# Kernel optimization log

Measured on AMD Instinct MI355X. Metric: run time of the kernel, lower is better.

Reference implementation:

```python
import jax, jax.numpy as jnp
import numpy as np
import math

BS, LQ, LKV = 4, 2048, 2048
D_LATENT, D_MODEL, HEADS = 512, 512, 8
D_K = D_MODEL // HEADS


def setup_inputs() -> dict:
    key = jax.random.key(0)
    ks = jax.random.split(key, 12)
    s = 0.02
    return {
        "q": jax.random.normal(ks[0], (BS, LQ, D_LATENT), jnp.float32),
        "k": jax.random.normal(ks[1], (BS, LKV, D_MODEL), jnp.float32),
        "v": jax.random.normal(ks[2], (BS, LKV, D_MODEL), jnp.float32),
        "weights": jax.random.uniform(ks[3], (BS, LKV), jnp.float32) + 1e-3,
        "Wq": jax.random.normal(ks[4], (D_LATENT, D_MODEL), jnp.float32) * s,
        "bq": jnp.zeros((D_MODEL,), jnp.float32),
        "Wk": jax.random.normal(ks[5], (D_MODEL, D_MODEL), jnp.float32) * s,
        "bk": jnp.zeros((D_MODEL,), jnp.float32),
        "Wv": jax.random.normal(ks[6], (D_MODEL, D_MODEL), jnp.float32) * s,
        "bv": jnp.zeros((D_MODEL,), jnp.float32),
        "Wo": jax.random.normal(ks[7], (D_MODEL, D_MODEL), jnp.float32) * s,
        "bo": jnp.zeros((D_MODEL,), jnp.float32),
    }


def reference(q, k, v, weights, Wq, bq, Wk, bk, Wv, bv, Wo, bo):
    bs = q.shape[0]
    # QKV projections, split into heads: [bs, h, L, d_k]
    qh = (q @ Wq + bq).reshape(bs, -1, HEADS, D_K).transpose(0, 2, 1, 3)
    kh = (k @ Wk + bk).reshape(bs, -1, HEADS, D_K).transpose(0, 2, 1, 3)
    vh = (v @ Wv + bv).reshape(bs, -1, HEADS, D_K).transpose(0, 2, 1, 3)
    # scaled dot-product scores [bs, h, Lq, Lkv]
    scores = jnp.einsum("bhqd,bhkd->bhqk", qh, kh) / math.sqrt(D_K)
    p = jax.nn.softmax(scores, axis=-1)
    # post-softmax external weight renormalization
    wp = p * weights[:, None, None, :]
    wp = wp / wp.sum(-1, keepdims=True)
    out = jnp.einsum("bhqk,bhkd->bhqd", wp, vh)
    concat = out.transpose(0, 2, 1, 3).reshape(bs, -1, D_MODEL)
    return concat @ Wo + bo
```

## Files before the change

### kernel.cpp

```cpp
#include <hip/hip_runtime.h>
#include <hip/hip_bf16.h>

#define LQ 2048
#define LKV 2048
#define DM 512
#define NH 8
#define DK 64

typedef __attribute__((ext_vector_type(8))) __bf16 bf16x8;
typedef __attribute__((ext_vector_type(4))) float f32x4;
typedef __attribute__((ext_vector_type(16))) float f32x16;

#define AS1 __attribute__((address_space(1)))
#define AS3 __attribute__((address_space(3)))

static __device__ __forceinline__ unsigned short f2bf(float x) {
  unsigned u = __float_as_uint(x);
  return (unsigned short)((u + 0x7fffu + ((u >> 16) & 1u)) >> 16);
}
static __device__ __forceinline__ float bf2f(unsigned short u) {
  return __uint_as_float(((unsigned)u) << 16);
}
static __device__ __forceinline__ bf16x8 cvt8(f32x4 a, f32x4 b) {
  bf16x8 r;
  r[0] = (__bf16)a[0]; r[1] = (__bf16)a[1]; r[2] = (__bf16)a[2]; r[3] = (__bf16)a[3];
  r[4] = (__bf16)b[0]; r[5] = (__bf16)b[1]; r[6] = (__bf16)b[2]; r[7] = (__bf16)b[3];
  return r;
}

__global__ __launch_bounds__(256) void transpose_w(
    const float* __restrict__ Wq, const float* __restrict__ Wk,
    const float* __restrict__ Wv, const float* __restrict__ Wo,
    unsigned short* __restrict__ WtAll)
{
  const float* W = blockIdx.z == 0 ? Wq : blockIdx.z == 1 ? Wk : blockIdx.z == 2 ? Wv : Wo;
  unsigned short* Wt = WtAll + (size_t)blockIdx.z * DM * DM;
  __shared__ float tile[32][33];
  const int t = threadIdx.x;
  const int tr = t >> 3;
  const int tc4 = (t & 7) * 4;
  const int k0 = blockIdx.x * 32, n0 = blockIdx.y * 32;
  float4 v = *(const float4*)(W + (size_t)(k0 + tr) * DM + n0 + tc4);
  tile[tr][tc4 + 0] = v.x; tile[tr][tc4 + 1] = v.y;
  tile[tr][tc4 + 2] = v.z; tile[tr][tc4 + 3] = v.w;
  __syncthreads();
  ushort4 o;
  o.x = f2bf(tile[tc4 + 0][tr]);
  o.y = f2bf(tile[tc4 + 1][tr]);
  o.z = f2bf(tile[tc4 + 2][tr]);
  o.w = f2bf(tile[tc4 + 3][tr]);
  *(ushort4*)(Wt + (size_t)(n0 + tr) * DM + k0 + tc4) = o;
}

__global__ __launch_bounds__(256) void gemm_qkv(
    const float* __restrict__ qin, const float* __restrict__ kin, const float* __restrict__ vin,
    const unsigned short* __restrict__ WtAll,
    const float* __restrict__ bq, const float* __restrict__ bk, const float* __restrict__ bv,
    unsigned short* __restrict__ qh, unsigned short* __restrict__ kh, unsigned short* __restrict__ vh)
{
  const int bid = blockIdx.x;
  const int x = bid & 7, j = bid >> 3;
  const int p = x + 8 * (j >> 2);
  const int nt = j & 3;
  const int mode = p >> 6, mtile = p & 63;

  const float* A = mode == 0 ? qin : (mode == 1 ? kin : vin);
  const unsigned short* Bt = WtAll + (size_t)mode * DM * DM;
  const float* bias = mode == 0 ? bq : (mode == 1 ? bk : bv);
  unsigned short* out = mode == 0 ? qh : (mode == 1 ? kh : vh);
  const float scale = (mode == 0) ? 0.18033688011112042f : 1.0f;

  __shared__ __align__(16) float As[128 * 32];
  __shared__ __align__(16) unsigned short Bs[128 * 32];

  const int tid = threadIdx.x;
  const int lane = tid & 63;
  const int w = tid >> 6;
  const int wr = w >> 1, wc = w & 1;
  const int l15 = lane & 15, g = lane >> 4;
  const int m0 = mtile * 128, n0 = nt * 128;

  f32x4 acc[4][4] = {};

  for (int k0 = 0; k0 < DM; k0 += 32) {
#pragma unroll
    for (int i = 0; i < 4; ++i) {
      int c = tid + i * 256;
      int row = c >> 3, slot = c & 7;
      const float* src = A + (size_t)(m0 + row) * DM + k0 + ((slot ^ (row & 7)) << 2);
      __builtin_amdgcn_global_load_lds((const AS1 unsigned*)src,
                                       (AS3 unsigned*)((char*)As + c * 16), 16, 0, 0);
    }
#pragma unroll
    for (int i = 0; i < 2; ++i) {
      int c = tid + i * 256;
      int row = c >> 2, slot = c & 3;
      const unsigned short* src = Bt + (size_t)(n0 + row) * DM + k0 + ((slot ^ ((row >> 1) & 3)) * 8);
      __builtin_amdgcn_global_load_lds((const AS1 unsigned*)src,
                                       (AS3 unsigned*)((char*)Bs + c * 16), 16, 0, 0);
    }
    __syncthreads();

    bf16x8 af[4], bfr[4];
#pragma unroll
    for (int mi = 0; mi < 4; ++mi) {
      int row = wr * 64 + mi * 16 + l15;
      f32x4 a0 = *(const f32x4*)((const char*)As + row * 128 + (((2 * g) ^ (row & 7)) << 4));
      f32x4 a1 = *(const f32x4*)((const char*)As + row * 128 + (((2 * g + 1) ^ (row & 7)) << 4));
      af[mi] = cvt8(a0, a1);
    }
#pragma unroll
    for (int ni = 0; ni < 4; ++ni) {
      int row = wc * 64 + ni * 16 + l15;
      bfr[ni] = *(const bf16x8*)((const char*)Bs + row * 64 + ((g ^ ((row >> 1) & 3)) * 16));
    }
#pragma unroll
    for (int mi = 0; mi < 4; ++mi)
#pragma unroll
      for (int ni = 0; ni < 4; ++ni)
        acc[mi][ni] = __builtin_amdgcn_mfma_f32_16x16x32_bf16(af[mi], bfr[ni], acc[mi][ni], 0, 0, 0);
    __syncthreads();
  }

#pragma unroll
  for (int mi = 0; mi < 4; ++mi) {
#pragma unroll
    for (int ni = 0; ni < 4; ++ni) {
      int n = n0 + wc * 64 + ni * 16 + l15;
      float bs = bias[n];
      int h = n >> 6, d = n & 63;
#pragma unroll
      for (int r = 0; r < 4; ++r) {
        int m = m0 + wr * 64 + mi * 16 + g * 4 + r;
        int b = m >> 11, li = m & 2047;
        float val = (acc[mi][ni][r] + bs) * scale;
        out[(((size_t)(b * NH + h)) * LQ + li) * DK + d] = f2bf(val);
      }
    }
  }
}

__global__ __launch_bounds__(256) void gemm_out(
    const unsigned short* __restrict__ A, const unsigned short* __restrict__ Bt,
    const float* __restrict__ bias, float* __restrict__ out)
{
  __shared__ __align__(16) unsigned short Al[128 * 40];
  __shared__ __align__(16) unsigned short Bl[128 * 40];
  const int tid = threadIdx.x;
  const int lane = tid & 63;
  const int w = tid >> 6;
  const int wr = w >> 1, wc = w & 1;
  const int l15 = lane & 15, g = lane >> 4;
  const int m0 = blockIdx.x * 128, n0 = blockIdx.y * 128;
  f32x4 acc[4][4] = {};

  for (int k0 = 0; k0 < DM; k0 += 32) {
#pragma unroll
    for (int i = 0; i < 2; ++i) {
      int idx = tid + i * 256;
      int row = idx >> 2, seg = idx & 3;
      *(int4*)(&Al[row * 40 + seg * 8]) =
          *(const int4*)(A + (size_t)(m0 + row) * DM + k0 + seg * 8);
      *(int4*)(&Bl[row * 40 + seg * 8]) =
          *(const int4*)(Bt + (size_t)(n0 + row) * DM + k0 + seg * 8);
    }
    __syncthreads();
    bf16x8 af[4], bfr[4];
#pragma unroll
    for (int mi = 0; mi < 4; ++mi)
      af[mi] = *(const bf16x8*)(&Al[(wr * 64 + mi * 16 + l15) * 40 + g * 8]);
#pragma unroll
    for (int ni = 0; ni < 4; ++ni)
      bfr[ni] = *(const bf16x8*)(&Bl[(wc * 64 + ni * 16 + l15) * 40 + g * 8]);
#pragma unroll
    for (int mi = 0; mi < 4; ++mi)
#pragma unroll
      for (int ni = 0; ni < 4; ++ni)
        acc[mi][ni] = __builtin_amdgcn_mfma_f32_16x16x32_bf16(af[mi], bfr[ni], acc[mi][ni], 0, 0, 0);
    __syncthreads();
  }

#pragma unroll
  for (int mi = 0; mi < 4; ++mi) {
#pragma unroll
    for (int ni = 0; ni < 4; ++ni) {
      int n = n0 + wc * 64 + ni * 16 + l15;
      float bs = bias[n];
#pragma unroll
      for (int r = 0; r < 4; ++r) {
        int m = m0 + wr * 64 + mi * 16 + g * 4 + r;
        out[(size_t)m * DM + n] = acc[mi][ni][r] + bs;
      }
    }
  }
}

__global__ __launch_bounds__(256) void prep_kv(
    const unsigned short* __restrict__ kh, const unsigned short* __restrict__ vh,
    const float* __restrict__ wts,
    unsigned short* __restrict__ kf, unsigned short* __restrict__ vf,
    unsigned short* __restrict__ wbf)
{
  __shared__ __align__(16) unsigned short t[64 * 72];
  const int bh = blockIdx.y, l0 = blockIdx.x * 64;
  const int b = bh >> 3;
  const size_t base = (size_t)bh * LKV * DK;
  const int tid = threadIdx.x;

  if ((bh & 7) == 0 && tid < 64) {
    int kv = l0 + tid;
    int r = kv & 15;
    int p = (r & 3) | ((r & 4) << 1) | ((r & 8) >> 1);
    wbf[b * LKV + (kv & ~15) + p] = f2bf(wts[b * LKV + kv]);
  }

#pragma unroll
  for (int i = 0; i < 2; ++i) {
    int c = tid + i * 256;
    int sl = c & 63, cq = (c >> 6) & 3, tl = c >> 8;
    int kv = tl * 32 + (sl & 31);
    int4 blk = *(const int4*)(kh + base + (size_t)(l0 + kv) * DK + cq * 16 + (sl >> 5) * 8);
    *(int4*)(kf + base + ((((size_t)(l0 >> 5) + tl) * 4 + cq) * 64 + sl) * 8) = blk;
  }

#pragma unroll
  for (int i = 0; i < 2; ++i) {
    int idx = tid + i * 256;
    int row = idx >> 3, seg = idx & 7;
    *(int4*)(&t[row * 72 + seg * 8]) =
        *(const int4*)(vh + base + (size_t)(l0 + row) * DK + seg * 8);
  }
  __syncthreads();
#pragma unroll
  for (int i = 0; i < 2; ++i) {
    int idx = tid + i * 256;
    int d = idx >> 3, seg = idx & 7;
    int kvg = l0 + seg * 8;
    float4 wa = *(const float4*)(wts + b * LKV + kvg);
    float4 wb4 = *(const float4*)(wts + b * LKV + kvg + 4);
    unsigned short r0 = f2bf(wa.x * bf2f(t[(seg * 8 + 0) * 72 + d]));
    unsigned short r1 = f2bf(wa.y * bf2f(t[(seg * 8 + 1) * 72 + d]));
    unsigned short r2 = f2bf(wa.z * bf2f(t[(seg * 8 + 2) * 72 + d]));
    unsigned short r3 = f2bf(wa.w * bf2f(t[(seg * 8 + 3) * 72 + d]));
    unsigned short r4 = f2bf(wb4.x * bf2f(t[(seg * 8 + 4) * 72 + d]));
    unsigned short r5 = f2bf(wb4.y * bf2f(t[(seg * 8 + 5) * 72 + d]));
    unsigned short r6 = f2bf(wb4.z * bf2f(t[(seg * 8 + 6) * 72 + d]));
    unsigned short r7 = f2bf(wb4.w * bf2f(t[(seg * 8 + 7) * 72 + d]));
    int T = kvg >> 4, s = (kvg >> 3) & 1, dh = d >> 5, dl = d & 31;
    size_t slot = (((size_t)bh * 128 + T) * 2 + dh) * 64;
    ushort4 lo4, hi4;
    lo4.x = r0; lo4.y = r1; lo4.z = r2; lo4.w = r3;
    hi4.x = r4; hi4.y = r5; hi4.z = r6; hi4.w = r7;
    *(ushort4*)(vf + (slot + dl) * 8 + 4 * s) = lo4;
    *(ushort4*)(vf + (slot + dl + 32) * 8 + 4 * s) = hi4;
  }
}

__global__ __launch_bounds__(512, 4) void attn_fwd(
    const unsigned short* __restrict__ qh, const unsigned short* __restrict__ kf,
    const unsigned short* __restrict__ vf, const unsigned short* __restrict__ wbf,
    unsigned short* __restrict__ ao)
{
  const int bid = blockIdx.x;
  const int xcd = bid & 7, wi = bid >> 3;
  const int bh = xcd * 4 + (wi >> 4);
  const int qb = wi & 15;
  const int b = bh >> 3, h = bh & 7;
  const int tid = threadIdx.x, lane = tid & 63, w = tid >> 6;
  const int wq = w & 3, half = w >> 2;
  const int l31 = lane & 31, hi = lane >> 5;

  __shared__ __align__(16) char smem[36928];

  const size_t kv_bh = (size_t)bh * (LKV * DK);
  const unsigned short* kfb = kf + kv_bh;
  const unsigned short* vfb = vf + kv_bh;

  const int q0 = qb * 128 + wq * 32;

#define STAGE(buf, t)                                                                     \
  do {                                                                                    \
    int tg_ = half * 32 + (t);                                                            \
    const unsigned short* ks_ = kfb + ((size_t)(tg_ * 4 + wq) * 64 + lane) * 8;           \
    const unsigned short* vs_ = vfb + ((size_t)((tg_ * 2 + (wq >> 1)) * 2 + (wq & 1)) * 64 + lane) * 8; \
    char* kd_ = smem + (buf) * 16384 + half * 8192 + wq * 1024;                           \
    char* vd_ = smem + (buf) * 16384 + half * 8192 + 4096 + wq * 1024;                    \
    __builtin_amdgcn_global_load_lds((const AS1 unsigned*)ks_, (AS3 unsigned*)kd_, 16, 0, 0); \
    __builtin_amdgcn_global_load_lds((const AS1 unsigned*)vs_, (AS3 unsigned*)vd_, 16, 0, 0); \
  } while (0)

  if (tid < 256)
    __builtin_amdgcn_global_load_lds((const AS1 unsigned*)(wbf + b * LKV + tid * 8),
                                     (AS3 unsigned*)(smem + 32768 + tid * 16), 16, 0, 0);
  if (tid < 16) *(int*)(smem + 36864 + tid * 4) = 0;
  STAGE(0, 0);

  bf16x8 qf[4];
  {
    const unsigned short* qp = qh + kv_bh + (size_t)(q0 + l31) * DK + hi * 8;
#pragma unroll
    for (int cq = 0; cq < 4; ++cq) qf[cq] = *(const bf16x8*)(qp + cq * 16);
  }
  __syncthreads();

  const char* wl = smem + 32768 + half * 2048 + hi * 16;
  const char* zpad = smem + 36864;
  f32x16 accO0 = {}, accO1 = {}, accL = {};
  int cur = 0;

#pragma unroll 2
  for (int t = 0; t < 32; ++t) {
    if (t < 31) {
      STAGE(cur ^ 1, t + 1);
      asm volatile("s_waitcnt vmcnt(2)" ::: "memory");
    } else {
      asm volatile("s_waitcnt vmcnt(0)" ::: "memory");
    }
    __builtin_amdgcn_s_barrier();

    const char* Kb = smem + cur * 16384 + half * 8192;
    const char* Vb = Kb + 4096;

    __builtin_amdgcn_s_setprio(1);
    f32x16 s = {};
#pragma unroll
    for (int cq = 0; cq < 4; ++cq) {
      bf16x8 kfr = *(const bf16x8*)(Kb + cq * 1024 + lane * 16);
      s = __builtin_amdgcn_mfma_f32_32x32x16_bf16(kfr, qf[cq], s, 0, 0, 0);
    }

    union { unsigned u[8]; bf16x8 v[2]; } P;
#pragma unroll
    for (int r2 = 0; r2 < 8; ++r2) {
      float lo = __builtin_amdgcn_exp2f(s[2 * r2]);
      float hv = __builtin_amdgcn_exp2f(s[2 * r2 + 1]);
      __bf16 bl = (__bf16)lo, bh2 = (__bf16)hv;
      unsigned short ul = __builtin_bit_cast(unsigned short, bl);
      unsigned short uh = __builtin_bit_cast(unsigned short, bh2);
      P.u[r2] = (unsigned)ul | ((unsigned)uh << 16);
    }

    const char* wsel = (l31 == 0) ? (wl + t * 64) : zpad;

#pragma unroll
    for (int c = 0; c < 2; ++c) {
      bf16x8 vb0 = *(const bf16x8*)(Vb + (c * 2 + 0) * 1024 + lane * 16);
      bf16x8 vb1 = *(const bf16x8*)(Vb + (c * 2 + 1) * 1024 + lane * 16);
      bf16x8 wb = *(const bf16x8*)(wsel + c * 32);

      accO0 = __builtin_amdgcn_mfma_f32_32x32x16_bf16(P.v[c], vb0, accO0, 0, 0, 0);
      accO1 = __builtin_amdgcn_mfma_f32_32x32x16_bf16(P.v[c], vb1, accO1, 0, 0, 0);
      accL  = __builtin_amdgcn_mfma_f32_32x32x16_bf16(P.v[c], wb,  accL,  0, 0, 0);
    }
    __builtin_amdgcn_s_setprio(0);

    asm volatile("s_waitcnt lgkmcnt(0)" ::: "memory");
    __builtin_amdgcn_s_barrier();
    cur ^= 1;
  }
#undef STAGE

  float* Ob = (float*)smem;
  float* Lb = (float*)(smem + 34816);
  if (half == 1) {
#pragma unroll
    for (int r = 0; r < 16; ++r) {
      int qp_ = (r & 3) + 8 * (r >> 2) + 4 * hi;
      Ob[(wq * 32 + qp_) * 68 + l31] = accO0[r];
      Ob[(wq * 32 + qp_) * 68 + 32 + l31] = accO1[r];
    }
    if (l31 == 0) {
#pragma unroll
      for (int r = 0; r < 16; ++r) {
        int qp_ = (r & 3) + 8 * (r >> 2) + 4 * hi;
        Lb[wq * 32 + qp_] = accL[r];
      }
    }
  }
  __syncthreads();
  if (half == 0) {
#pragma unroll
    for (int r = 0; r < 16; ++r) {
      int qp_ = (r & 3) + 8 * (r >> 2) + 4 * hi;
      float L = __shfl(accL[r], lane & 32) + Lb[wq * 32 + qp_];
      float inv = 1.0f / L;
      float o0 = accO0[r] + Ob[(wq * 32 + qp_) * 68 + l31];
      float o1 = accO1[r] + Ob[(wq * 32 + qp_) * 68 + 32 + l31];
      size_t off = ((size_t)(b * LQ + q0 + qp_)) * DM + h * DK;
      ao[off + l31] = f2bf(o0 * inv);
      ao[off + 32 + l31] = f2bf(o1 * inv);
    }
  }
}

extern "C" void kernel_launch(void* const* d_in, const int* in_sizes, int n_in,
                              void* d_out, int out_size, void* d_ws, size_t ws_size,
                              hipStream_t stream)
{
  const float* q  = (const float*)d_in[0];
  const float* k  = (const float*)d_in[1];
  const float* v  = (const float*)d_in[2];
  const float* wt = (const float*)d_in[3];
  const float* Wq = (const float*)d_in[4];
  const float* bq = (const float*)d_in[5];
  const float* Wk = (const float*)d_in[6];
  const float* bk = (const float*)d_in[7];
  const float* Wv = (const float*)d_in[8];
  const float* bv = (const float*)d_in[9];
  const float* Wo = (const float*)d_in[10];
  const float* bo = (const float*)d_in[11];

  char* ws = (char*)d_ws;
  unsigned short* qh = (unsigned short*)(ws + 0);
  unsigned short* kfr= (unsigned short*)(ws + 8388608);
  unsigned short* vfr= (unsigned short*)(ws + 16777216);
  unsigned short* ao = (unsigned short*)(ws + 25165824);
  unsigned short* Wt = (unsigned short*)(ws + 33554432);
  unsigned short* vh = (unsigned short*)(ws + 35651584);
  unsigned short* wbf= (unsigned short*)(ws + 44040192);
  unsigned short* kh = ao;

  transpose_w<<<dim3(16, 16, 4), 256, 0, stream>>>(Wq, Wk, Wv, Wo, Wt);
  gemm_qkv<<<768, 256, 0, stream>>>(q, k, v, Wt, bq, bk, bv, qh, kh, vh);
  prep_kv<<<dim3(32, 32), 256, 0, stream>>>(kh, vh, wt, kfr, vfr, wbf);
  attn_fwd<<<512, 512, 0, stream>>>(qh, kfr, vfr, wbf, ao);
  gemm_out<<<dim3(64, 4), 256, 0, stream>>>(ao, Wt + 3 * (size_t)DM * DM, bo, (float*)d_out);
}
```

Before: 95.70 us.

## Load V fragments directly into registers and swizzle output-GEMM LDS via direct loads

In the attention kernel, V tiles are no longer staged through LDS. Each wave loads its own V fragments straight from global memory into registers at the start of each iteration, which halves the LDS ring and relies on the wave-specific V layout. The waitcnt counts are adjusted to account for the extra outstanding loads. The output GEMM switches to global_load_lds with an XOR-swizzled, unpadded LDS layout, which removes the register round trip and the padding. The risk is exposed global load latency for V, since it is fetched only one iteration ahead, and a smaller LDS footprint that may change occupancy.

```diff
diff --git a/kernel.cpp b/kernel.cpp
--- a/kernel.cpp
+++ b/kernel.cpp
@@ -144,8 +144,8 @@
     const unsigned short* __restrict__ A, const unsigned short* __restrict__ Bt,
     const float* __restrict__ bias, float* __restrict__ out)
 {
-  __shared__ __align__(16) unsigned short Al[128 * 40];
-  __shared__ __align__(16) unsigned short Bl[128 * 40];
+  __shared__ __align__(16) unsigned short Al[128 * 32];
+  __shared__ __align__(16) unsigned short Bl[128 * 32];
   const int tid = threadIdx.x;
   const int lane = tid & 63;
   const int w = tid >> 6;
@@ -157,21 +157,28 @@
   for (int k0 = 0; k0 < DM; k0 += 32) {
 #pragma unroll
     for (int i = 0; i < 2; ++i) {
-      int idx = tid + i * 256;
-      int row = idx >> 2, seg = idx & 3;
-      *(int4*)(&Al[row * 40 + seg * 8]) =
-          *(const int4*)(A + (size_t)(m0 + row) * DM + k0 + seg * 8);
-      *(int4*)(&Bl[row * 40 + seg * 8]) =
-          *(const int4*)(Bt + (size_t)(n0 + row) * DM + k0 + seg * 8);
+      int c = tid + i * 256;
+      int row = c >> 2, slot = c & 3;
+      int so = (slot ^ ((row >> 1) & 3)) * 8;
+      __builtin_amdgcn_global_load_lds(
+          (const AS1 unsigned*)(A + (size_t)(m0 + row) * DM + k0 + so),
+          (AS3 unsigned*)((char*)Al + c * 16), 16, 0, 0);
+      __builtin_amdgcn_global_load_lds(
+          (const AS1 unsigned*)(Bt + (size_t)(n0 + row) * DM + k0 + so),
+          (AS3 unsigned*)((char*)Bl + c * 16), 16, 0, 0);
     }
     __syncthreads();
     bf16x8 af[4], bfr[4];
 #pragma unroll
-    for (int mi = 0; mi < 4; ++mi)
-      af[mi] = *(const bf16x8*)(&Al[(wr * 64 + mi * 16 + l15) * 40 + g * 8]);
-#pragma unroll
-    for (int ni = 0; ni < 4; ++ni)
-      bfr[ni] = *(const bf16x8*)(&Bl[(wc * 64 + ni * 16 + l15) * 40 + g * 8]);
+    for (int mi = 0; mi < 4; ++mi) {
+      int row = wr * 64 + mi * 16 + l15;
+      af[mi] = *(const bf16x8*)((const char*)Al + row * 64 + ((g ^ ((row >> 1) & 3)) * 16));
+    }
+#pragma unroll
+    for (int ni = 0; ni < 4; ++ni) {
+      int row = wc * 64 + ni * 16 + l15;
+      bfr[ni] = *(const bf16x8*)((const char*)Bl + row * 64 + ((g ^ ((row >> 1) & 3)) * 16));
+    }
 #pragma unroll
     for (int mi = 0; mi < 4; ++mi)
 #pragma unroll
@@ -270,7 +277,7 @@
   const int wq = w & 3, half = w >> 2;
   const int l31 = lane & 31, hi = lane >> 5;
 
-  __shared__ __align__(16) char smem[36928];
+  __shared__ __align__(16) char smem[35328];
 
   const size_t kv_bh = (size_t)bh * (LKV * DK);
   const unsigned short* kfb = kf + kv_bh;
@@ -282,17 +289,14 @@
   do {                                                                                    \
     int tg_ = half * 32 + (t);                                                            \
     const unsigned short* ks_ = kfb + ((size_t)(tg_ * 4 + wq) * 64 + lane) * 8;           \
-    const unsigned short* vs_ = vfb + ((size_t)((tg_ * 2 + (wq >> 1)) * 2 + (wq & 1)) * 64 + lane) * 8; \
-    char* kd_ = smem + (buf) * 16384 + half * 8192 + wq * 1024;                           \
-    char* vd_ = smem + (buf) * 16384 + half * 8192 + 4096 + wq * 1024;                    \
+    char* kd_ = smem + (buf) * 8192 + half * 4096 + wq * 1024;                            \
     __builtin_amdgcn_global_load_lds((const AS1 unsigned*)ks_, (AS3 unsigned*)kd_, 16, 0, 0); \
-    __builtin_amdgcn_global_load_lds((const AS1 unsigned*)vs_, (AS3 unsigned*)vd_, 16, 0, 0); \
   } while (0)
 
   if (tid < 256)
     __builtin_amdgcn_global_load_lds((const AS1 unsigned*)(wbf + b * LKV + tid * 8),
-                                     (AS3 unsigned*)(smem + 32768 + tid * 16), 16, 0, 0);
-  if (tid < 16) *(int*)(smem + 36864 + tid * 4) = 0;
+                                     (AS3 unsigned*)(smem + 16384 + tid * 16), 16, 0, 0);
+  if (tid < 16) *(int*)(smem + 20480 + tid * 4) = 0;
   STAGE(0, 0);
 
   bf16x8 qf[4];
@@ -303,23 +307,30 @@
   }
   __syncthreads();
 
-  const char* wl = smem + 32768 + half * 2048 + hi * 16;
-  const char* zpad = smem + 36864;
+  const char* wl = smem + 16384 + half * 2048 + hi * 16;
+  const char* zpad = smem + 20480;
   f32x16 accO0 = {}, accO1 = {}, accL = {};
   int cur = 0;
 
 #pragma unroll 2
   for (int t = 0; t < 32; ++t) {
+    const int tg = half * 32 + t;
+
+    const unsigned short* vt_ = vfb + ((size_t)tg << 11) + lane * 8;
+    bf16x8 vbr0 = *(const bf16x8*)(vt_);
+    bf16x8 vbr1 = *(const bf16x8*)(vt_ + 512);
+    bf16x8 vbr2 = *(const bf16x8*)(vt_ + 1024);
+    bf16x8 vbr3 = *(const bf16x8*)(vt_ + 1536);
+
     if (t < 31) {
       STAGE(cur ^ 1, t + 1);
-      asm volatile("s_waitcnt vmcnt(2)" ::: "memory");
+      asm volatile("s_waitcnt vmcnt(5)" ::: "memory");
     } else {
-      asm volatile("s_waitcnt vmcnt(0)" ::: "memory");
+      asm volatile("s_waitcnt vmcnt(4)" ::: "memory");
     }
     __builtin_amdgcn_s_barrier();
 
-    const char* Kb = smem + cur * 16384 + half * 8192;
-    const char* Vb = Kb + 4096;
+    const char* Kb = smem + cur * 8192 + half * 4096;
 
     __builtin_amdgcn_s_setprio(1);
     f32x16 s = {};
@@ -342,15 +353,15 @@
 
     const char* wsel = (l31 == 0) ? (wl + t * 64) : zpad;
 
-#pragma unroll
-    for (int c = 0; c < 2; ++c) {
-      bf16x8 vb0 = *(const bf16x8*)(Vb + (c * 2 + 0) * 1024 + lane * 16);
-      bf16x8 vb1 = *(const bf16x8*)(Vb + (c * 2 + 1) * 1024 + lane * 16);
-      bf16x8 wb = *(const bf16x8*)(wsel + c * 32);
-
-      accO0 = __builtin_amdgcn_mfma_f32_32x32x16_bf16(P.v[c], vb0, accO0, 0, 0, 0);
-      accO1 = __builtin_amdgcn_mfma_f32_32x32x16_bf16(P.v[c], vb1, accO1, 0, 0, 0);
-      accL  = __builtin_amdgcn_mfma_f32_32x32x16_bf16(P.v[c], wb,  accL,  0, 0, 0);
+    {
+      bf16x8 wb0 = *(const bf16x8*)(wsel);
+      bf16x8 wb1 = *(const bf16x8*)(wsel + 32);
+      accO0 = __builtin_amdgcn_mfma_f32_32x32x16_bf16(P.v[0], vbr0, accO0, 0, 0, 0);
+      accO1 = __builtin_amdgcn_mfma_f32_32x32x16_bf16(P.v[0], vbr1, accO1, 0, 0, 0);
+      accL  = __builtin_amdgcn_mfma_f32_32x32x16_bf16(P.v[0], wb0,  accL,  0, 0, 0);
+      accO0 = __builtin_amdgcn_mfma_f32_32x32x16_bf16(P.v[1], vbr2, accO0, 0, 0, 0);
+      accO1 = __builtin_amdgcn_mfma_f32_32x32x16_bf16(P.v[1], vbr3, accO1, 0, 0, 0);
+      accL  = __builtin_amdgcn_mfma_f32_32x32x16_bf16(P.v[1], wb1,  accL,  0, 0, 0);
     }
     __builtin_amdgcn_s_setprio(0);
 
```

Result: no change. 96.21 us (+0.5%).

## Fuse K/V fragment relayout and weight scaling into QKV GEMM epilogue

Applied to the files above, without the earlier changes.

Removes the separate prep_kv kernel. The QKV GEMM epilogue now stages K and V tiles in shared memory and writes them straight into the attention fragment layouts, and folds the per-key weight multiply into V. The bf16 conversion of the weights moves into the weight-transpose kernel. This saves one launch and a full round trip of K/V through global memory, at the cost of a longer epilogue with extra syncs. The gemm_out kernel also switches to direct global-to-LDS loads with an XOR swizzle instead of a padded LDS layout.

```diff
diff --git a/kernel.cpp b/kernel.cpp
--- a/kernel.cpp
+++ b/kernel.cpp
@@ -18,9 +18,6 @@
   unsigned u = __float_as_uint(x);
   return (unsigned short)((u + 0x7fffu + ((u >> 16) & 1u)) >> 16);
 }
-static __device__ __forceinline__ float bf2f(unsigned short u) {
-  return __uint_as_float(((unsigned)u) << 16);
-}
 static __device__ __forceinline__ bf16x8 cvt8(f32x4 a, f32x4 b) {
   bf16x8 r;
   r[0] = (__bf16)a[0]; r[1] = (__bf16)a[1]; r[2] = (__bf16)a[2]; r[3] = (__bf16)a[3];
@@ -31,12 +28,23 @@
 __global__ __launch_bounds__(256) void transpose_w(
     const float* __restrict__ Wq, const float* __restrict__ Wk,
     const float* __restrict__ Wv, const float* __restrict__ Wo,
-    unsigned short* __restrict__ WtAll)
+    const float* __restrict__ wts,
+    unsigned short* __restrict__ WtAll, unsigned short* __restrict__ wbf)
 {
   const float* W = blockIdx.z == 0 ? Wq : blockIdx.z == 1 ? Wk : blockIdx.z == 2 ? Wv : Wo;
   unsigned short* Wt = WtAll + (size_t)blockIdx.z * DM * DM;
   __shared__ float tile[32][33];
   const int t = threadIdx.x;
+  if (blockIdx.z == 0 && blockIdx.y == 0) {
+    int idx = blockIdx.x * 512 + t * 2;
+#pragma unroll
+    for (int i = 0; i < 2; ++i) {
+      int kv = idx + i;
+      int r = kv & 15;
+      int ph = (r & 3) | ((r & 4) << 1) | ((r & 8) >> 1);
+      wbf[(kv & ~15) | ph] = f2bf(wts[kv]);
+    }
+  }
   const int tr = t >> 3;
   const int tc4 = (t & 7) * 4;
   const int k0 = blockIdx.x * 32, n0 = blockIdx.y * 32;
@@ -56,22 +64,23 @@
     const float* __restrict__ qin, const float* __restrict__ kin, const float* __restrict__ vin,
     const unsigned short* __restrict__ WtAll,
     const float* __restrict__ bq, const float* __restrict__ bk, const float* __restrict__ bv,
-    unsigned short* __restrict__ qh, unsigned short* __restrict__ kh, unsigned short* __restrict__ vh)
+    const float* __restrict__ wts,
+    unsigned short* __restrict__ qh, unsigned short* __restrict__ kf, unsigned short* __restrict__ vf)
 {
   const int bid = blockIdx.x;
   const int x = bid & 7, j = bid >> 3;
-  const int p = x + 8 * (j >> 2);
+  const int p_ = x + 8 * (j >> 2);
   const int nt = j & 3;
-  const int mode = p >> 6, mtile = p & 63;
+  const int mode = p_ >> 6, mtile = p_ & 63;
 
   const float* A = mode == 0 ? qin : (mode == 1 ? kin : vin);
   const unsigned short* Bt = WtAll + (size_t)mode * DM * DM;
   const float* bias = mode == 0 ? bq : (mode == 1 ? bk : bv);
-  unsigned short* out = mode == 0 ? qh : (mode == 1 ? kh : vh);
   const float scale = (mode == 0) ? 0.18033688011112042f : 1.0f;
 
-  __shared__ __align__(16) float As[128 * 32];
-  __shared__ __align__(16) unsigned short Bs[128 * 32];
+  __shared__ __align__(16) char sm[24576];
+  float* As = (float*)sm;
+  unsigned short* Bs = (unsigned short*)(sm + 16384);
 
   const int tid = threadIdx.x;
   const int lane = tid & 63;
@@ -122,19 +131,98 @@
     __syncthreads();
   }
 
-#pragma unroll
-  for (int mi = 0; mi < 4; ++mi) {
-#pragma unroll
-    for (int ni = 0; ni < 4; ++ni) {
-      int n = n0 + wc * 64 + ni * 16 + l15;
-      float bs = bias[n];
-      int h = n >> 6, d = n & 63;
-#pragma unroll
-      for (int r = 0; r < 4; ++r) {
-        int m = m0 + wr * 64 + mi * 16 + g * 4 + r;
-        int b = m >> 11, li = m & 2047;
-        float val = (acc[mi][ni][r] + bs) * scale;
-        out[(((size_t)(b * NH + h)) * LQ + li) * DK + d] = f2bf(val);
+  if (mode == 0) {
+#pragma unroll
+    for (int mi = 0; mi < 4; ++mi) {
+#pragma unroll
+      for (int ni = 0; ni < 4; ++ni) {
+        int n = n0 + wc * 64 + ni * 16 + l15;
+        float bs = bias[n];
+        int h = n >> 6, d = n & 63;
+#pragma unroll
+        for (int r = 0; r < 4; ++r) {
+          int m = m0 + wr * 64 + mi * 16 + g * 4 + r;
+          int b = m >> 11, li = m & 2047;
+          qh[(((size_t)(b * NH + h)) * LQ + li) * DK + d] = f2bf((acc[mi][ni][r] + bs) * scale);
+        }
+      }
+    }
+  } else if (mode == 1) {
+    unsigned short* tile = (unsigned short*)sm;
+    const int b = m0 >> 11;
+    const int kv0 = m0 & 2047;
+#pragma unroll
+    for (int p = 0; p < 2; ++p) {
+      __syncthreads();
+      if (wc == p) {
+#pragma unroll
+        for (int mi = 0; mi < 4; ++mi)
+#pragma unroll
+          for (int ni = 0; ni < 4; ++ni) {
+            float bs = bias[n0 + p * 64 + ni * 16 + l15];
+#pragma unroll
+            for (int r = 0; r < 4; ++r)
+              tile[(wr * 64 + mi * 16 + g * 4 + r) * 72 + ni * 16 + l15] =
+                  f2bf(acc[mi][ni][r] + bs);
+          }
+      }
+      __syncthreads();
+      int h = (n0 >> 6) + p;
+      const size_t basebh = (size_t)(b * NH + h) * (LKV * DK);
+#pragma unroll
+      for (int i = 0; i < 4; ++i) {
+        int e = tid + i * 256;
+        int sl = e & 63, cq = (e >> 6) & 3, Tl = e >> 8;
+        int kvl = Tl * 32 + (sl & 31);
+        int s8 = cq * 2 + (sl >> 5);
+        int4 blk = *(const int4*)(tile + kvl * 72 + s8 * 8);
+        size_t T = (size_t)((kv0 >> 5) + Tl);
+        *(int4*)(kf + basebh + ((T * 4 + cq) * 64 + sl) * 8) = blk;
+      }
+    }
+  } else {
+    unsigned short* tile = (unsigned short*)sm;
+    const int b = m0 >> 11;
+    const int kv0 = m0 & 2047;
+    f32x4 wv[4];
+#pragma unroll
+    for (int mi = 0; mi < 4; ++mi)
+      wv[mi] = *(const f32x4*)(wts + b * LKV + kv0 + wr * 64 + mi * 16 + g * 4);
+#pragma unroll
+    for (int p = 0; p < 2; ++p) {
+      __syncthreads();
+      if (wc == p) {
+#pragma unroll
+        for (int mi = 0; mi < 4; ++mi)
+#pragma unroll
+          for (int ni = 0; ni < 4; ++ni) {
+            float bs = bias[n0 + p * 64 + ni * 16 + l15];
+            ushort4 pk;
+            pk.x = f2bf((acc[mi][ni][0] + bs) * wv[mi][0]);
+            pk.y = f2bf((acc[mi][ni][1] + bs) * wv[mi][1]);
+            pk.z = f2bf((acc[mi][ni][2] + bs) * wv[mi][2]);
+            pk.w = f2bf((acc[mi][ni][3] + bs) * wv[mi][3]);
+            *(ushort4*)(tile + (ni * 16 + l15) * 136 + wr * 64 + mi * 16 + g * 4) = pk;
+          }
+      }
+      __syncthreads();
+      int h = (n0 >> 6) + p;
+      const size_t basebh = (size_t)(b * NH + h) * (LKV * DK);
+#pragma unroll
+      for (int i = 0; i < 4; ++i) {
+        int e = tid + i * 256;
+        int lane64 = e & 63, dh = (e >> 6) & 1, Tl = e >> 7;
+        int d = dh * 32 + (lane64 & 31);
+        int kvb = Tl * 16 + (lane64 >> 5) * 4;
+        ushort4 lo = *(const ushort4*)(tile + d * 136 + kvb);
+        ushort4 hi = *(const ushort4*)(tile + d * 136 + kvb + 8);
+        int4 o;
+        o.x = (int)((unsigned)lo.x | ((unsigned)lo.y << 16));
+        o.y = (int)((unsigned)lo.z | ((unsigned)lo.w << 16));
+        o.z = (int)((unsigned)hi.x | ((unsigned)hi.y << 16));
+        o.w = (int)((unsigned)hi.z | ((unsigned)hi.w << 16));
+        size_t T = (size_t)((kv0 >> 4) + Tl);
+        *(int4*)(vf + basebh + ((T * 2 + dh) * 64 + lane64) * 8) = o;
       }
     }
   }
@@ -144,8 +232,8 @@
     const unsigned short* __restrict__ A, const unsigned short* __restrict__ Bt,
     const float* __restrict__ bias, float* __restrict__ out)
 {
-  __shared__ __align__(16) unsigned short Al[128 * 40];
-  __shared__ __align__(16) unsigned short Bl[128 * 40];
+  __shared__ __align__(16) unsigned short Al[128 * 32];
+  __shared__ __align__(16) unsigned short Bl[128 * 32];
   const int tid = threadIdx.x;
   const int lane = tid & 63;
   const int w = tid >> 6;
@@ -157,21 +245,28 @@
   for (int k0 = 0; k0 < DM; k0 += 32) {
 #pragma unroll
     for (int i = 0; i < 2; ++i) {
-      int idx = tid + i * 256;
-      int row = idx >> 2, seg = idx & 3;
-      *(int4*)(&Al[row * 40 + seg * 8]) =
-          *(const int4*)(A + (size_t)(m0 + row) * DM + k0 + seg * 8);
-      *(int4*)(&Bl[row * 40 + seg * 8]) =
-          *(const int4*)(Bt + (size_t)(n0 + row) * DM + k0 + seg * 8);
+      int c = tid + i * 256;
+      int row = c >> 2, slot = c & 3;
+      int so = (slot ^ ((row >> 1) & 3)) * 8;
+      __builtin_amdgcn_global_load_lds(
+          (const AS1 unsigned*)(A + (size_t)(m0 + row) * DM + k0 + so),
+          (AS3 unsigned*)((char*)Al + c * 16), 16, 0, 0);
+      __builtin_amdgcn_global_load_lds(
+          (const AS1 unsigned*)(Bt + (size_t)(n0 + row) * DM + k0 + so),
+          (AS3 unsigned*)((char*)Bl + c * 16), 16, 0, 0);
     }
     __syncthreads();
     bf16x8 af[4], bfr[4];
 #pragma unroll
-    for (int mi = 0; mi < 4; ++mi)
-      af[mi] = *(const bf16x8*)(&Al[(wr * 64 + mi * 16 + l15) * 40 + g * 8]);
-#pragma unroll
-    for (int ni = 0; ni < 4; ++ni)
-      bfr[ni] = *(const bf16x8*)(&Bl[(wc * 64 + ni * 16 + l15) * 40 + g * 8]);
+    for (int mi = 0; mi < 4; ++mi) {
+      int row = wr * 64 + mi * 16 + l15;
+      af[mi] = *(const bf16x8*)((const char*)Al + row * 64 + ((g ^ ((row >> 1) & 3)) * 16));
+    }
+#pragma unroll
+    for (int ni = 0; ni < 4; ++ni) {
+      int row = wc * 64 + ni * 16 + l15;
+      bfr[ni] = *(const bf16x8*)((const char*)Bl + row * 64 + ((g ^ ((row >> 1) & 3)) * 16));
+    }
 #pragma unroll
     for (int mi = 0; mi < 4; ++mi)
 #pragma unroll
@@ -192,67 +287,6 @@
         out[(size_t)m * DM + n] = acc[mi][ni][r] + bs;
       }
     }
-  }
-}
-
-__global__ __launch_bounds__(256) void prep_kv(
-    const unsigned short* __restrict__ kh, const unsigned short* __restrict__ vh,
-    const float* __restrict__ wts,
-    unsigned short* __restrict__ kf, unsigned short* __restrict__ vf,
-    unsigned short* __restrict__ wbf)
-{
-  __shared__ __align__(16) unsigned short t[64 * 72];
-  const int bh = blockIdx.y, l0 = blockIdx.x * 64;
-  const int b = bh >> 3;
-  const size_t base = (size_t)bh * LKV * DK;
-  const int tid = threadIdx.x;
-
-  if ((bh & 7) == 0 && tid < 64) {
-    int kv = l0 + tid;
-    int r = kv & 15;
-    int p = (r & 3) | ((r & 4) << 1) | ((r & 8) >> 1);
-    wbf[b * LKV + (kv & ~15) + p] = f2bf(wts[b * LKV + kv]);
-  }
-
-#pragma unroll
-  for (int i = 0; i < 2; ++i) {
-    int c = tid + i * 256;
-    int sl = c & 63, cq = (c >> 6) & 3, tl = c >> 8;
-    int kv = tl * 32 + (sl & 31);
-    int4 blk = *(const int4*)(kh + base + (size_t)(l0 + kv) * DK + cq * 16 + (sl >> 5) * 8);
-    *(int4*)(kf + base + ((((size_t)(l0 >> 5) + tl) * 4 + cq) * 64 + sl) * 8) = blk;
-  }
-
-#pragma unroll
-  for (int i = 0; i < 2; ++i) {
-    int idx = tid + i * 256;
-    int row = idx >> 3, seg = idx & 7;
-    *(int4*)(&t[row * 72 + seg * 8]) =
-        *(const int4*)(vh + base + (size_t)(l0 + row) * DK + seg * 8);
-  }
-  __syncthreads();
-#pragma unroll
-  for (int i = 0; i < 2; ++i) {
-    int idx = tid + i * 256;
-    int d = idx >> 3, seg = idx & 7;
-    int kvg = l0 + seg * 8;
-    float4 wa = *(const float4*)(wts + b * LKV + kvg);
-    float4 wb4 = *(const float4*)(wts + b * LKV + kvg + 4);
-    unsigned short r0 = f2bf(wa.x * bf2f(t[(seg * 8 + 0) * 72 + d]));
-    unsigned short r1 = f2bf(wa.y * bf2f(t[(seg * 8 + 1) * 72 + d]));
-    unsigned short r2 = f2bf(wa.z * bf2f(t[(seg * 8 + 2) * 72 + d]));
-    unsigned short r3 = f2bf(wa.w * bf2f(t[(seg * 8 + 3) * 72 + d]));
-    unsigned short r4 = f2bf(wb4.x * bf2f(t[(seg * 8 + 4) * 72 + d]));
-    unsigned short r5 = f2bf(wb4.y * bf2f(t[(seg * 8 + 5) * 72 + d]));
-    unsigned short r6 = f2bf(wb4.z * bf2f(t[(seg * 8 + 6) * 72 + d]));
-    unsigned short r7 = f2bf(wb4.w * bf2f(t[(seg * 8 + 7) * 72 + d]));
-    int T = kvg >> 4, s = (kvg >> 3) & 1, dh = d >> 5, dl = d & 31;
-    size_t slot = (((size_t)bh * 128 + T) * 2 + dh) * 64;
-    ushort4 lo4, hi4;
-    lo4.x = r0; lo4.y = r1; lo4.z = r2; lo4.w = r3;
-    hi4.x = r4; hi4.y = r5; hi4.z = r6; hi4.w = r7;
-    *(ushort4*)(vf + (slot + dl) * 8 + 4 * s) = lo4;
-    *(ushort4*)(vf + (slot + dl + 32) * 8 + 4 * s) = hi4;
   }
 }
 
@@ -416,13 +450,10 @@
   unsigned short* vfr= (unsigned short*)(ws + 16777216);
   unsigned short* ao = (unsigned short*)(ws + 25165824);
   unsigned short* Wt = (unsigned short*)(ws + 33554432);
-  unsigned short* vh = (unsigned short*)(ws + 35651584);
   unsigned short* wbf= (unsigned short*)(ws + 44040192);
-  unsigned short* kh = ao;
-
-  transpose_w<<<dim3(16, 16, 4), 256, 0, stream>>>(Wq, Wk, Wv, Wo, Wt);
-  gemm_qkv<<<768, 256, 0, stream>>>(q, k, v, Wt, bq, bk, bv, qh, kh, vh);
-  prep_kv<<<dim3(32, 32), 256, 0, stream>>>(kh, vh, wt, kfr, vfr, wbf);
+
+  transpose_w<<<dim3(16, 16, 4), 256, 0, stream>>>(Wq, Wk, Wv, Wo, wt, Wt, wbf);
+  gemm_qkv<<<768, 256, 0, stream>>>(q, k, v, Wt, bq, bk, bv, wt, qh, kfr, vfr);
   attn_fwd<<<512, 512, 0, stream>>>(qh, kfr, vfr, wbf, ao);
   gemm_out<<<dim3(64, 4), 256, 0, stream>>>(ao, Wt + 3 * (size_t)DM * DM, bo, (float*)d_out);
 }
```

After: 114.7 us. +19.8%, slower.
